# Optimization experiments

Measured on AMD Instinct MI355X. Metric: run time of the kernel, lower is better.

Reference implementation:

```python
import jax, jax.numpy as jnp
import numpy as np
import math

N_HEAD = 16


def setup_inputs() -> dict:
    key = jax.random.key(0)
    ks = jax.random.split(key, 9)
    B, T, D = 2, 2048, 1024
    s = 1.0 / math.sqrt(D)
    return {
        "queries": jax.random.normal(ks[0], (B, T, D), jnp.float32),
        "keys": jax.random.normal(ks[1], (B, T, D), jnp.float32),
        "key_mask": jax.random.randint(ks[2], (B, T), 0, 2, jnp.int32),
        "Wq": jax.random.normal(ks[3], (D, D), jnp.float32) * s,
        "bq": jax.random.normal(ks[4], (D,), jnp.float32) * 0.01,
        "Wk": jax.random.normal(ks[5], (D, D), jnp.float32) * s,
        "bk": jax.random.normal(ks[6], (D,), jnp.float32) * 0.01,
        "Wv": jax.random.normal(ks[7], (D, D), jnp.float32) * s,
        "bv": jax.random.normal(ks[8], (D,), jnp.float32) * 0.01,
    }


def reference(queries, keys, key_mask, Wq, bq, Wk, bk, Wv, bv):
    B, Tq, D = queries.shape
    Tk = keys.shape[1]
    H = N_HEAD
    dk = D // H
    scale = 1.0 / math.sqrt(dk)

    # torch Linear: x @ W.T + b
    Q = (queries @ Wq.T + bq).reshape(B, Tq, H, dk)
    K = (keys @ Wk.T + bk).reshape(B, Tk, H, dk)
    V = (keys @ Wv.T + bv).reshape(B, Tk, H, dk)

    # flatten batch-major over (B, H) to match torch permute+reshape -> (B*H, T, dk)
    Qf = Q.transpose(0, 2, 1, 3).reshape(B * H, Tq, dk)
    Kf = K.transpose(0, 2, 1, 3).reshape(B * H, Tk, dk)
    Vf = V.transpose(0, 2, 1, 3).reshape(B * H, Tk, dk)

    scores = jnp.einsum("nqd,nkd->nqk", Qf, Kf) * scale  # (B*H, Tq, Tk)

    # torch builds masks via .repeat(n_head,1,1): HEAD-major tiling (H copies of B).
    # flat row i of scores has batch i//H but receives mask of batch i%B —
    # reproduced faithfully here.
    km = jnp.tile(key_mask, (H, 1))  # (H*B, Tk), row j -> key_mask[j % B]
    scores = jnp.where(km[:, None, :] == 0, -1e9, scores)

    attn = jax.nn.softmax(scores, axis=-1)
    qm = jnp.tile(key_mask, (H, 1))[:, :, None].astype(attn.dtype)  # (H*B, Tk, 1), Tq==Tk
    attn = attn * qm

    # dropout: identity in eval mode
    out = jnp.einsum("nqk,nkd->nqd", attn, Vf)  # (B*H, Tq, dk)
    out = out.reshape(B, H, Tq, dk).transpose(0, 2, 1, 3).reshape(B, Tq, D)
    return out
```

## Files before the change

kernel.cpp:

```cpp
#include <hip/hip_runtime.h>
#include <hip/hip_bf16.h>

typedef __attribute__((ext_vector_type(8))) short bf16x8;
typedef __attribute__((ext_vector_type(4))) short bf16x4;
typedef __attribute__((ext_vector_type(4))) float f32x4;
typedef __attribute__((ext_vector_type(16))) float f32x16;
typedef __attribute__((ext_vector_type(4))) unsigned u32x4;

__device__ inline short f2bf(float f) {
    unsigned u = __builtin_bit_cast(unsigned, f);
    u += 0x7FFF + ((u >> 16) & 1);
    return (short)(u >> 16);
}


__global__ __launch_bounds__(256) void cvt_bf16(
    const float* __restrict__ xq, const float* __restrict__ xk,
    const float* __restrict__ Wq, const float* __restrict__ Wk,
    const float* __restrict__ Wv, const int* __restrict__ key_mask,
    short* __restrict__ ws)
{
    const int blk = blockIdx.x;
    if (blk >= 11264) {
        float* bias = (float*)(ws + 24117248u);
        const int i0 = threadIdx.x * 4;
#pragma unroll
        for (int p = 0; p < 4; ++p) {
            int idx = p * 1024 + i0;
            int4 m = *(const int4*)&key_mask[idx];
            f32x4 o = { m.x ? 0.f : -1e9f, m.y ? 0.f : -1e9f,
                        m.z ? 0.f : -1e9f, m.w ? 0.f : -1e9f };
            *(f32x4*)&bias[idx] = o;
        }
        return;
    }
    int seg, local;
    if (blk < 4096)      { seg = 0; local = blk; }
    else if (blk < 8192) { seg = 1; local = blk - 4096; }
    else                 { seg = 2 + ((blk - 8192) >> 10); local = (blk - 8192) & 1023; }
    const float* src = (seg == 0) ? xq : (seg == 1) ? xk
                     : (seg == 2) ? Wq : (seg == 3) ? Wk : Wv;
    const size_t dstoff = (seg == 0) ? 12582912u : (seg == 1) ? 16777216u
                        : 20971520u + (size_t)(seg - 2) * 1048576u;
    const size_t idx = (size_t)local * 1024 + threadIdx.x * 4;
    float4 v = *(const float4*)&src[idx];
    bf16x4 o = { f2bf(v.x), f2bf(v.y), f2bf(v.z), f2bf(v.w) };
    *(bf16x4*)&ws[dstoff + idx] = o;
}

__global__ __launch_bounds__(256) void proj_gemm(
    short* __restrict__ ws, const float* __restrict__ bq,
    const float* __restrict__ bk, const float* __restrict__ bv)
{
    const int z = blockIdx.z;
    const short* A  = ws + ((z == 0) ? 12582912u : 16777216u);
    const short* Bw = ws + 20971520u + (size_t)z * 1048576u;
    const float* bias = (z == 0) ? bq : (z == 1) ? bk : bv;
    short* out = ws + (size_t)z * 4194304u;

    const int m0 = blockIdx.x * 128;
    const int n0 = blockIdx.y * 128;
    const int tid  = threadIdx.x;
    const int lane = tid & 63;
    const int wid  = tid >> 6;
    const int wr = wid >> 1, wc = wid & 1;
    const int l15 = lane & 15, lhi = lane >> 4;

    __shared__ alignas(16) short SM[24576];

    const int srow = wid * 32 + (lane >> 2);
    const int scol = (lane & 3) * 8;
    const short* aSrc = A  + (size_t)(m0 + srow) * 1024 + scol;
    const short* bSrc = Bw + (size_t)(n0 + srow) * 1024 + scol;

#define PSTAGE(T, BUF) do {                                                    \
    _Pragma("unroll")                                                          \
    for (int i_ = 0; i_ < 2; ++i_) {                                           \
        __builtin_amdgcn_global_load_lds(                                      \
            (const __attribute__((address_space(1))) unsigned*)                \
                (aSrc + (T) * 32 + i_ * 16384),                                \
            (__attribute__((address_space(3))) unsigned*)                      \
                &SM[(BUF) * 8192 + (wid * 32 + i_ * 16) * 32], 16, 0, 0);      \
        __builtin_amdgcn_global_load_lds(                                      \
            (const __attribute__((address_space(1))) unsigned*)                \
                (bSrc + (T) * 32 + i_ * 16384),                                \
            (__attribute__((address_space(3))) unsigned*)                      \
                &SM[(BUF) * 8192 + 4096 + (wid * 32 + i_ * 16) * 32], 16, 0, 0);\
    } } while (0)

    f32x4 acc[4][4] = {};

    PSTAGE(0, 0);
    PSTAGE(1, 1);
    for (int t = 0; t < 32; ++t) {
        const int buf = t % 3;
        if (t < 31) {
            asm volatile("s_waitcnt vmcnt(4)" ::: "memory");
        } else {
            asm volatile("s_waitcnt vmcnt(0)" ::: "memory");
        }
        __builtin_amdgcn_s_barrier();
        __builtin_amdgcn_sched_barrier(0);
        if (t < 30) PSTAGE(t + 2, (t + 2) % 3);

        const short* SA = &SM[buf * 8192];
        const short* SB = SA + 4096;
        bf16x8 a[4], b[4];
#pragma unroll
        for (int i = 0; i < 4; ++i)
            a[i] = *(const bf16x8*)&SA[(wr * 64 + i * 16 + l15) * 32 + lhi * 8];
#pragma unroll
        for (int j = 0; j < 4; ++j)
            b[j] = *(const bf16x8*)&SB[(wc * 64 + j * 16 + l15) * 32 + lhi * 8];

        if (z == 2) {
#pragma unroll
            for (int i = 0; i < 4; ++i)
#pragma unroll
                for (int j = 0; j < 4; ++j)
                    acc[i][j] = __builtin_amdgcn_mfma_f32_16x16x32_bf16(
                        a[i], b[j], acc[i][j], 0, 0, 0);
        } else {
#pragma unroll
            for (int i = 0; i < 4; ++i)
#pragma unroll
                for (int j = 0; j < 4; ++j)
                    acc[i][j] = __builtin_amdgcn_mfma_f32_16x16x32_bf16(
                        b[j], a[i], acc[i][j], 0, 0, 0);
        }
    }
#undef PSTAGE

    __syncthreads();
    if (z == 2) {
#pragma unroll
        for (int i = 0; i < 4; ++i) {
            int mm = wr * 64 + i * 16 + lhi * 4;
#pragma unroll
            for (int j = 0; j < 4; ++j) {
                int nn = wc * 64 + j * 16 + l15;
                float bval = bias[n0 + nn];
                bf16x4 pk = { f2bf(acc[i][j][0] + bval), f2bf(acc[i][j][1] + bval),
                              f2bf(acc[i][j][2] + bval), f2bf(acc[i][j][3] + bval) };
                *(bf16x4*)&SM[nn * 136 + mm] = pk;
            }
        }
    } else {
#pragma unroll
        for (int i = 0; i < 4; ++i) {
            int mm = wr * 64 + i * 16 + l15;
#pragma unroll
            for (int j = 0; j < 4; ++j) {
                int nnb = wc * 64 + j * 16 + lhi * 4;
                float4 bw = *(const float4*)&bias[n0 + nnb];
                bf16x4 pk = { f2bf(acc[i][j][0] + bw.x), f2bf(acc[i][j][1] + bw.y),
                              f2bf(acc[i][j][2] + bw.z), f2bf(acc[i][j][3] + bw.w) };
                *(bf16x4*)&SM[mm * 136 + nnb] = pk;
            }
        }
    }
    __syncthreads();

    const int bb = m0 >> 11;
    const int mt = m0 & 2047;
#pragma unroll
    for (int p = 0; p < 8; ++p) {
        int id = p * 256 + tid;
        int rr = id >> 4;
        int g  = id & 15;
        bf16x8 v = *(const bf16x8*)&SM[rr * 136 + g * 8];
        if (z == 2) {
            int nn = n0 + rr, h = nn >> 6, d = nn & 63;
            *(bf16x8*)&out[(((size_t)(bb * 16 + h)) * 64 + d) * 2048 + mt + g * 8] = v;
        } else {
            int nn = n0 + g * 8, h = nn >> 6, d = nn & 63;
            *(bf16x8*)&out[(((size_t)(bb * 16 + h)) * 2048 + mt + rr) * 64 + d] = v;
        }
    }
}

__device__ inline float pair_max(float v) { return fmaxf(v, __shfl_xor(v, 32)); }
__device__ inline float pair_sum(float v) { return v + __shfl_xor(v, 32); }

__global__ __launch_bounds__(512, 4) void attn_fwd(
    const short* __restrict__ Qb, const short* __restrict__ Kb,
    const short* __restrict__ Vtb, const int* __restrict__ key_mask,
    const float* __restrict__ biasArr, float* __restrict__ out)
{
    const int bh = blockIdx.x;
    const int qb = blockIdx.y;
    const int b  = bh >> 4;
    const int h  = bh & 15;
    const int mb = bh & 1;
    const int tid  = threadIdx.x;
    const int lane = tid & 63;
    const int wid  = tid >> 6;
    const int qg   = wid & 3;
    const int ks   = wid >> 2;
    const int l31  = lane & 31;
    const int hi   = lane >> 5;

    const size_t base = (size_t)bh * 2048 * 64;
    const int q0 = qb * 128 + qg * 32;
    const int ko = ks * 1024;

    __shared__ alignas(16) char SMEM[65536];
    short* KVbase = (short*)SMEM + ks * 16384;
#define KVS(BUF) (KVbase + (BUF) * 8192)

    const int* km_row = key_mask + mb * 2048;
    const float* bias_row = biasArr + mb * 2048;

    bf16x8 qf[4];
#pragma unroll
    for (int kf = 0; kf < 4; ++kf)
        qf[kf] = *(const bf16x8*)&Qb[base + (size_t)(q0 + l31) * 64 + kf * 16 + hi * 8];

    const int lrow = lane >> 3;
    const int lcol = (lane & 7) ^ (lrow & 7);
    const short* srcK[2];
    const short* srcV[2];
#pragma unroll
    for (int i = 0; i < 2; ++i) {
        int r0 = qg * 16 + i * 8;
        srcK[i] = Kb  + base + (size_t)(ko + r0 + lrow) * 64 + lcol * 8;
        srcV[i] = Vtb + base + (size_t)(r0 + lrow) * 2048 + ko + lcol * 8;
    }

    f32x16 acc[2];
#pragma unroll
    for (int n = 0; n < 2; ++n)
#pragma unroll
        for (int r = 0; r < 16; ++r) acc[n][r] = 0.f;
    float mrun = -1e30f, lrun = 0.f;
    const float SC  = 0.18033688f;
    const float DTH = 44.3614f;

#define STAGE(T, BUF)                                                          \
    {                                                                          \
        _Pragma("unroll")                                                      \
        for (int i = 0; i < 2; ++i) {                                          \
            int r0 = qg * 16 + i * 8;                                          \
            __builtin_amdgcn_global_load_lds(                                  \
                (const __attribute__((address_space(1))) unsigned int*)        \
                    (srcK[i] + (size_t)(T) * 4096),                            \
                (__attribute__((address_space(3))) unsigned int*)              \
                    &KVS(BUF)[r0 * 64],                                        \
                16, 0, 0);                                                     \
            __builtin_amdgcn_global_load_lds(                                  \
                (const __attribute__((address_space(1))) unsigned int*)        \
                    (srcV[i] + (size_t)(T) * 64),                              \
                (__attribute__((address_space(3))) unsigned int*)              \
                    &KVS(BUF)[4096 + r0 * 64],                                 \
                16, 0, 0);                                                     \
        }                                                                      \
    }

    STAGE(0, 0);

    for (int t = 0; t < 16; ++t) {
        const int buf = t & 1;
        const int k0 = ko + t * 64;
        __syncthreads();
        if (t < 15) STAGE(t + 1, buf ^ 1);

        const f32x4* bp = (const f32x4*)(bias_row + k0);
        f32x16 sacc[2];
#pragma unroll
        for (int s = 0; s < 2; ++s) {
#pragma unroll
            for (int g = 0; g < 4; ++g) {
                f32x4 bv = bp[s * 8 + g * 2 + hi];
#pragma unroll
                for (int c = 0; c < 4; ++c) sacc[s][g * 4 + c] = bv[c];
            }
        }
        __builtin_amdgcn_s_setprio(1);
#pragma unroll
        for (int s = 0; s < 2; ++s) {
#pragma unroll
            for (int kf = 0; kf < 4; ++kf) {
                int row = s * 32 + l31;
                int xg = ((2 * kf + hi) ^ (row & 7)) * 8;
                bf16x8 kfr = *(const bf16x8*)&KVS(buf)[row * 64 + xg];
                sacc[s] = __builtin_amdgcn_mfma_f32_32x32x16_bf16(
                    kfr, qf[kf], sacc[s], 0, 0, 0);
            }
        }
        __builtin_amdgcn_s_setprio(0);

        float tm[16];
#pragma unroll
        for (int i = 0; i < 16; ++i) tm[i] = fmaxf(sacc[0][i], sacc[1][i]);
#pragma unroll
        for (int st = 8; st >= 1; st >>= 1)
#pragma unroll
            for (int i = 0; i < st; ++i) tm[i] = fmaxf(tm[i], tm[i + st]);
        float mx = pair_max(tm[0]);

        if (!__all(mx <= mrun + DTH)) {
            float mnew = fmaxf(mrun, mx);
            float fac  = __builtin_amdgcn_exp2f((mrun - mnew) * SC);
            lrun *= fac;
#pragma unroll
            for (int n = 0; n < 2; ++n)
#pragma unroll
                for (int r = 0; r < 16; ++r) acc[n][r] *= fac;
            mrun = mnew;
        }
        const float msc = mrun * SC;

        float p[2][16];
#pragma unroll
        for (int s = 0; s < 2; ++s)
#pragma unroll
            for (int r = 0; r < 16; ++r)
                p[s][r] = __builtin_amdgcn_exp2f(sacc[s][r] * SC - msc);

        float tsum[16];
#pragma unroll
        for (int i = 0; i < 16; ++i) tsum[i] = p[0][i] + p[1][i];
#pragma unroll
        for (int st = 8; st >= 1; st >>= 1)
#pragma unroll
            for (int i = 0; i < st; ++i) tsum[i] += tsum[i + st];
        lrun += pair_sum(tsum[0]);

        unsigned pk2[2][4][2];
#pragma unroll
        for (int s = 0; s < 2; ++s)
#pragma unroll
            for (int g = 0; g < 4; ++g)
#pragma unroll
                for (int w = 0; w < 2; ++w) {
                    unsigned d;
                    asm("v_cvt_pk_bf16_f32 %0, %1, %2"
                        : "=v"(d)
                        : "v"(p[s][g * 4 + 2 * w]), "v"(p[s][g * 4 + 2 * w + 1]));
                    pk2[s][g][w] = d;
                }

        __builtin_amdgcn_s_setprio(1);
#pragma unroll
        for (int s = 0; s < 2; ++s)
#pragma unroll
            for (int kk = 0; kk < 2; ++kk) {
                unsigned w0 = pk2[s][2 * kk][0],     w1 = pk2[s][2 * kk][1];
                unsigned w2 = pk2[s][2 * kk + 1][0], w3 = pk2[s][2 * kk + 1][1];
                asm("v_permlane32_swap_b32 %0, %1" : "+v"(w0), "+v"(w2));
                asm("v_permlane32_swap_b32 %0, %1" : "+v"(w1), "+v"(w3));
                u32x4 fv = { w0, w1, w2, w3 };
                bf16x8 pf = __builtin_bit_cast(bf16x8, fv);
                int kq = s * 2 + kk;
#pragma unroll
                for (int n = 0; n < 2; ++n) {
                    int row = n * 32 + l31;
                    int xg = ((2 * kq + hi) ^ (row & 7)) * 8;
                    bf16x8 vf = *(const bf16x8*)&KVS(buf)[4096 + row * 64 + xg];
                    acc[n] = __builtin_amdgcn_mfma_f32_32x32x16_bf16(
                        vf, pf, acc[n], 0, 0, 0);
                }
            }
        __builtin_amdgcn_s_setprio(0);
    }
#undef STAGE
#undef KVS

    __syncthreads();
    float* R = (float*)SMEM + qg * 2176;

    if (ks == 1) {
#pragma unroll
        for (int n = 0; n < 2; ++n)
#pragma unroll
            for (int r = 0; r < 16; ++r) {
                int d = n * 32 + (r & 3) + 8 * (r >> 2) + 4 * hi;
                R[d * 32 + l31] = acc[n][r];
            }
        if (hi == 0) { R[2048 + l31] = mrun; R[2080 + l31] = lrun; }
    }
    __syncthreads();

    if (ks == 0) {
        float m1 = R[2048 + l31];
        float l1 = R[2080 + l31];
        float o1[2][16];
#pragma unroll
        for (int n = 0; n < 2; ++n)
#pragma unroll
            for (int r = 0; r < 16; ++r) {
                int d = n * 32 + (r & 3) + 8 * (r >> 2) + 4 * hi;
                o1[n][r] = R[d * 32 + l31];
            }
        float mm = fmaxf(mrun, m1);
        float f0 = __builtin_amdgcn_exp2f((mrun - mm) * SC);
        float f1 = __builtin_amdgcn_exp2f((m1 - mm) * SC);
        float lt = lrun * f0 + l1 * f1;
        float qn = (float)km_row[q0 + l31] / lt;

#pragma unroll
        for (int n = 0; n < 2; ++n)
#pragma unroll
            for (int r = 0; r < 16; ++r) {
                int d = n * 32 + (r & 3) + 8 * (r >> 2) + 4 * hi;
                R[l31 * 68 + d] = (acc[n][r] * f0 + o1[n][r] * f1) * qn;
            }
        const int l15 = lane & 15, lq = lane >> 4;
#pragma unroll
        for (int rep = 0; rep < 8; ++rep) {
            int qr = rep * 4 + lq;
            f32x4 v = *(const f32x4*)&R[qr * 68 + l15 * 4];
            *(f32x4*)&out[((size_t)b * 2048 + q0 + qr) * 1024 + h * 64 + l15 * 4] = v;
        }
    }
}

extern "C" void kernel_launch(void* const* d_in, const int* in_sizes, int n_in,
                              void* d_out, int out_size, void* d_ws, size_t ws_size,
                              hipStream_t stream) {
    const float* queries = (const float*)d_in[0];
    const float* keys    = (const float*)d_in[1];
    const int*   key_mask= (const int*)d_in[2];
    const float* Wq = (const float*)d_in[3];
    const float* bq = (const float*)d_in[4];
    const float* Wk = (const float*)d_in[5];
    const float* bk = (const float*)d_in[6];
    const float* Wv = (const float*)d_in[7];
    const float* bv = (const float*)d_in[8];
    float* out = (float*)d_out;

    short* ws = (short*)d_ws;
    const float* biasArr = (const float*)(ws + 24117248u);

    cvt_bf16<<<11265, 256, 0, stream>>>(queries, keys, Wq, Wk, Wv, key_mask, ws);

    proj_gemm<<<dim3(32, 8, 3), 256, 0, stream>>>(ws, bq, bk, bv);

    attn_fwd<<<dim3(32, 16), 512, 0, stream>>>(
        ws, ws + 4194304, ws + 2 * 4194304, key_mask, biasArr, out);
}
```

Before: 122.2 us.

## Restructure projection GEMM to two waves with register-staged double-buffered LDS

The projection GEMM moves from four waves on 2x2 64x64 warp tiles to two waves, each computing a 64x128 tile. This raises the MFMA-to-LDS-read ratio per wave. The direct global-to-LDS triple-buffered loads become register-staged global loads, written into a padded, double-buffered LDS layout with a row stride of 40 to avoid bank conflicts. The idea is to cut LDS traffic and bank conflicts, at the cost of more registers per wave, fewer waves to hide latency, and a full vmcnt(0) wait every iteration.

```diff
diff --git a/kernel.cpp b/kernel.cpp
--- a/kernel.cpp
+++ b/kernel.cpp
@@ -48,7 +48,7 @@
     *(bf16x4*)&ws[dstoff + idx] = o;
 }
 
-__global__ __launch_bounds__(256) void proj_gemm(
+__global__ __launch_bounds__(128, 2) void proj_gemm(
     short* __restrict__ ws, const float* __restrict__ bq,
     const float* __restrict__ bk, const float* __restrict__ bv)
 {
@@ -63,82 +63,94 @@
     const int tid  = threadIdx.x;
     const int lane = tid & 63;
     const int wid  = tid >> 6;
-    const int wr = wid >> 1, wc = wid & 1;
     const int l15 = lane & 15, lhi = lane >> 4;
 
-    __shared__ alignas(16) short SM[24576];
-
-    const int srow = wid * 32 + (lane >> 2);
-    const int scol = (lane & 3) * 8;
-    const short* aSrc = A  + (size_t)(m0 + srow) * 1024 + scol;
-    const short* bSrc = Bw + (size_t)(n0 + srow) * 1024 + scol;
-
-#define PSTAGE(T, BUF) do {                                                    \
+    __shared__ alignas(16) short SM[20480];
+
+    const int srow = tid >> 2;
+    const int scol = (tid & 3) * 8;
+    const short* aS = A  + (size_t)(m0 + srow) * 1024 + scol;
+    const short* bS = Bw + (size_t)(n0 + srow) * 1024 + scol;
+    const int ldso = srow * 40 + scol;
+
+    bf16x8 stA[4], stB[4];
+
+#define LOADT(T) do {                                                          \
     _Pragma("unroll")                                                          \
-    for (int i_ = 0; i_ < 2; ++i_) {                                           \
-        __builtin_amdgcn_global_load_lds(                                      \
-            (const __attribute__((address_space(1))) unsigned*)                \
-                (aSrc + (T) * 32 + i_ * 16384),                                \
-            (__attribute__((address_space(3))) unsigned*)                      \
-                &SM[(BUF) * 8192 + (wid * 32 + i_ * 16) * 32], 16, 0, 0);      \
-        __builtin_amdgcn_global_load_lds(                                      \
-            (const __attribute__((address_space(1))) unsigned*)                \
-                (bSrc + (T) * 32 + i_ * 16384),                                \
-            (__attribute__((address_space(3))) unsigned*)                      \
-                &SM[(BUF) * 8192 + 4096 + (wid * 32 + i_ * 16) * 32], 16, 0, 0);\
+    for (int i_ = 0; i_ < 4; ++i_) {                                           \
+        stA[i_] = *(const bf16x8*)(aS + (T) * 32 + i_ * 32768);                \
+        stB[i_] = *(const bf16x8*)(bS + (T) * 32 + i_ * 32768);                \
     } } while (0)
 
-    f32x4 acc[4][4] = {};
-
-    PSTAGE(0, 0);
-    PSTAGE(1, 1);
+#define WRITES(BUF) do {                                                       \
+    short* wp_ = SM + (BUF) * 10240;                                           \
+    _Pragma("unroll")                                                          \
+    for (int i_ = 0; i_ < 4; ++i_) {                                           \
+        *(bf16x8*)(wp_ + ldso + i_ * 1280) = stA[i_];                          \
+        *(bf16x8*)(wp_ + 5120 + ldso + i_ * 1280) = stB[i_];                   \
+    } } while (0)
+
+    f32x4 acc[4][8] = {};
+
+    LOADT(0);
+    asm volatile("s_waitcnt vmcnt(0)" ::: "memory");
+    WRITES(0);
+    LOADT(1);
+    asm volatile("s_waitcnt lgkmcnt(0)" ::: "memory");
+    __builtin_amdgcn_s_barrier();
+    __builtin_amdgcn_sched_barrier(0);
+
     for (int t = 0; t < 32; ++t) {
-        const int buf = t % 3;
+        const short* SA = SM + (t & 1) * 10240;
+        const short* SB = SA + 5120;
+
+        bf16x8 a[4], b[8];
+#pragma unroll
+        for (int i = 0; i < 4; ++i)
+            a[i] = *(const bf16x8*)&SA[(wid * 64 + i * 16 + l15) * 40 + lhi * 8];
+#pragma unroll
+        for (int j = 0; j < 8; ++j)
+            b[j] = *(const bf16x8*)&SB[(j * 16 + l15) * 40 + lhi * 8];
+
         if (t < 31) {
-            asm volatile("s_waitcnt vmcnt(4)" ::: "memory");
-        } else {
             asm volatile("s_waitcnt vmcnt(0)" ::: "memory");
-        }
-        __builtin_amdgcn_s_barrier();
-        __builtin_amdgcn_sched_barrier(0);
-        if (t < 30) PSTAGE(t + 2, (t + 2) % 3);
-
-        const short* SA = &SM[buf * 8192];
-        const short* SB = SA + 4096;
-        bf16x8 a[4], b[4];
-#pragma unroll
-        for (int i = 0; i < 4; ++i)
-            a[i] = *(const bf16x8*)&SA[(wr * 64 + i * 16 + l15) * 32 + lhi * 8];
-#pragma unroll
-        for (int j = 0; j < 4; ++j)
-            b[j] = *(const bf16x8*)&SB[(wc * 64 + j * 16 + l15) * 32 + lhi * 8];
+            WRITES((t + 1) & 1);
+            if (t < 30) LOADT(t + 2);
+        }
 
         if (z == 2) {
 #pragma unroll
             for (int i = 0; i < 4; ++i)
 #pragma unroll
-                for (int j = 0; j < 4; ++j)
+                for (int j = 0; j < 8; ++j)
                     acc[i][j] = __builtin_amdgcn_mfma_f32_16x16x32_bf16(
                         a[i], b[j], acc[i][j], 0, 0, 0);
         } else {
 #pragma unroll
             for (int i = 0; i < 4; ++i)
 #pragma unroll
-                for (int j = 0; j < 4; ++j)
+                for (int j = 0; j < 8; ++j)
                     acc[i][j] = __builtin_amdgcn_mfma_f32_16x16x32_bf16(
                         b[j], a[i], acc[i][j], 0, 0, 0);
         }
-    }
-#undef PSTAGE
+
+        if (t < 31) {
+            asm volatile("s_waitcnt lgkmcnt(0)" ::: "memory");
+            __builtin_amdgcn_s_barrier();
+            __builtin_amdgcn_sched_barrier(0);
+        }
+    }
+#undef LOADT
+#undef WRITES
 
     __syncthreads();
     if (z == 2) {
 #pragma unroll
         for (int i = 0; i < 4; ++i) {
-            int mm = wr * 64 + i * 16 + lhi * 4;
-#pragma unroll
-            for (int j = 0; j < 4; ++j) {
-                int nn = wc * 64 + j * 16 + l15;
+            int mm = wid * 64 + i * 16 + lhi * 4;
+#pragma unroll
+            for (int j = 0; j < 8; ++j) {
+                int nn = j * 16 + l15;
                 float bval = bias[n0 + nn];
                 bf16x4 pk = { f2bf(acc[i][j][0] + bval), f2bf(acc[i][j][1] + bval),
                               f2bf(acc[i][j][2] + bval), f2bf(acc[i][j][3] + bval) };
@@ -148,10 +160,10 @@
     } else {
 #pragma unroll
         for (int i = 0; i < 4; ++i) {
-            int mm = wr * 64 + i * 16 + l15;
-#pragma unroll
-            for (int j = 0; j < 4; ++j) {
-                int nnb = wc * 64 + j * 16 + lhi * 4;
+            int mm = wid * 64 + i * 16 + l15;
+#pragma unroll
+            for (int j = 0; j < 8; ++j) {
+                int nnb = j * 16 + lhi * 4;
                 float4 bw = *(const float4*)&bias[n0 + nnb];
                 bf16x4 pk = { f2bf(acc[i][j][0] + bw.x), f2bf(acc[i][j][1] + bw.y),
                               f2bf(acc[i][j][2] + bw.z), f2bf(acc[i][j][3] + bw.w) };
@@ -164,8 +176,8 @@
     const int bb = m0 >> 11;
     const int mt = m0 & 2047;
 #pragma unroll
-    for (int p = 0; p < 8; ++p) {
-        int id = p * 256 + tid;
+    for (int p = 0; p < 16; ++p) {
+        int id = p * 128 + tid;
         int rr = id >> 4;
         int g  = id & 15;
         bf16x8 v = *(const bf16x8*)&SM[rr * 136 + g * 8];
@@ -434,7 +446,7 @@
 
     cvt_bf16<<<11265, 256, 0, stream>>>(queries, keys, Wq, Wk, Wv, key_mask, ws);
 
-    proj_gemm<<<dim3(32, 8, 3), 256, 0, stream>>>(ws, bq, bk, bv);
+    proj_gemm<<<dim3(32, 8, 3), 128, 0, stream>>>(ws, bq, bk, bv);
 
     attn_fwd<<<dim3(32, 16), 512, 0, stream>>>(
         ws, ws + 4194304, ws + 2 * 4194304, key_mask, biasArr, out);
```

Result: slower. 356.2 us (+191.5%).
